# Kernel optimization log

Measured on AMD Instinct MI355X. Metric: run time of the kernel, lower is better.

The kernel has to match this reference:

```python
import jax, jax.numpy as jnp
import numpy as np
import math

D_MODEL, N_HEADS, D_HEAD = 768, 12, 64
INIT_RANGE = 0.02
ROPE_BASE = 10000.0


def _rope_cos_sin(seq_len, d_head, dtype=jnp.float32):
    # theta_j = base^(-2j/d), positions m -> angles [T, d/2]
    inv_freq = 1.0 / (ROPE_BASE ** (jnp.arange(0, d_head, 2, dtype=jnp.float32) / d_head))
    ang = jnp.arange(seq_len, dtype=jnp.float32)[:, None] * inv_freq[None, :]
    return jnp.cos(ang).astype(dtype), jnp.sin(ang).astype(dtype)


def _apply_rope(x, cos, sin):
    # x: [b, t, h, d]; rotate consecutive (even, odd) pairs as complex numbers
    xr, xi = x[..., 0::2], x[..., 1::2]
    c = cos[None, :, None, :]
    s = sin[None, :, None, :]
    out_r = xr * c - xi * s
    out_i = xr * s + xi * c
    return jnp.stack([out_r, out_i], axis=-1).reshape(x.shape)


def setup_inputs() -> dict:
    key = jax.random.key(0)
    ks = jax.random.split(key, 5)
    B, T = 2, 2048
    x = jax.random.normal(ks[0], (B, T, D_MODEL), dtype=jnp.float32)
    W_Q = INIT_RANGE * jax.random.normal(ks[1], (N_HEADS, D_MODEL, D_HEAD), dtype=jnp.float32)
    W_K = INIT_RANGE * jax.random.normal(ks[2], (N_HEADS, D_MODEL, D_HEAD), dtype=jnp.float32)
    W_V = INIT_RANGE * jax.random.normal(ks[3], (N_HEADS, D_MODEL, D_HEAD), dtype=jnp.float32)
    W_O = INIT_RANGE * jax.random.normal(ks[4], (N_HEADS, D_HEAD, D_MODEL), dtype=jnp.float32)
    b_Q = jnp.zeros((N_HEADS, D_HEAD), dtype=jnp.float32)
    b_K = jnp.zeros((N_HEADS, D_HEAD), dtype=jnp.float32)
    b_V = jnp.zeros((N_HEADS, D_HEAD), dtype=jnp.float32)
    b_O = jnp.zeros((D_MODEL,), dtype=jnp.float32)
    return {"normalized_resid_pre": x, "W_Q": W_Q, "b_Q": b_Q, "W_K": W_K, "b_K": b_K,
            "W_V": W_V, "b_V": b_V, "W_O": W_O, "b_O": b_O}


def reference(normalized_resid_pre, W_Q, b_Q, W_K, b_K, W_V, b_V, W_O, b_O):
    x = normalized_resid_pre
    B, T, _ = x.shape
    cos, sin = _rope_cos_sin(T, D_HEAD, x.dtype)
    Q = jnp.einsum('btc,hcd->bthd', x, W_Q) + b_Q
    K = jnp.einsum('btc,hcd->bthd', x, W_K) + b_K
    V = jnp.einsum('btc,hcd->bthd', x, W_V) + b_V
    Q = _apply_rope(Q, cos, sin)
    K = _apply_rope(K, cos, sin)
    scores = jnp.einsum('bqhd,bkhd->bhqk', Q, K) / math.sqrt(D_HEAD)
    # Faithful to source: tril zeros upper triangle, then all exact zeros -> -inf
    tril = jnp.tril(jnp.ones((T, T), dtype=bool))
    z = jnp.where(tril[None, None], scores, 0.0)
    z = jnp.where(z == 0.0, -jnp.inf, z)
    probs = jax.nn.softmax(z, axis=-1)
    o = jnp.einsum('bhqk,bkhd->bqhd', probs, V)
    return jnp.einsum('bqhd,hdm->bqm', o, W_O) + b_O
```

## Files before the change

### kernel.cpp

```cpp
#include <hip/hip_runtime.h>

typedef unsigned short u16;
typedef unsigned int u32;
typedef short bf16x8 __attribute__((ext_vector_type(8)));
typedef float f32x4 __attribute__((ext_vector_type(4)));
typedef float f32x16 __attribute__((ext_vector_type(16)));

#define MFMA(a, b, c) __builtin_amdgcn_mfma_f32_16x16x32_bf16(a, b, c, 0, 0, 0)
#define MFMA32(a, b, c) __builtin_amdgcn_mfma_f32_32x32x16_bf16(a, b, c, 0, 0, 0)

__device__ __forceinline__ u16 f2bf(float f) {
  unsigned int u = __float_as_uint(f);
  u = (u + 0x7FFFu + ((u >> 16) & 1u)) >> 16;
  return (u16)u;
}

#define GLOAD16(gp, lp)                                                        \
  __builtin_amdgcn_global_load_lds(                                            \
      (const __attribute__((address_space(1))) void*)(gp),                     \
      (__attribute__((address_space(3))) void*)(lp), 16, 0, 0)


__global__ void rope_tables(float* __restrict__ cost, float* __restrict__ sint) {
  int idx = blockIdx.x * 256 + threadIdx.x;
  if (idx >= 2048 * 32) return;
  int t = idx >> 5, i = idx & 31;
  float invf = expf(-(float)i * 0.28782313662425572f);
  float ang = (float)t * invf;
  cost[idx] = cosf(ang);
  sint[idx] = sinf(ang);
}

__global__ void cast_x(const float* __restrict__ x, u16* __restrict__ xb, int n) {
  int i = (blockIdx.x * 256 + threadIdx.x) * 4;
  if (i >= n) return;
  float4 v = *(const float4*)(x + i);
  u16 o0 = f2bf(v.x), o1 = f2bf(v.y), o2 = f2bf(v.z), o3 = f2bf(v.w);
  ushort4 o = make_ushort4(o0, o1, o2, o3);
  *(ushort4*)(xb + i) = o;
}

__global__ void prep_wqkv(const float* __restrict__ WQ, const float* __restrict__ WK,
                          const float* __restrict__ WV, u16* __restrict__ Wt) {
  __shared__ float tile[32][33];
  const int z = blockIdx.z;
  const int qkv = z / 12, h = z - qkv * 12;
  const float* W = (qkv == 0 ? WQ : qkv == 1 ? WK : WV) + (size_t)h * 768 * 64;
  const int k0 = blockIdx.x * 32, d0 = blockIdx.y * 32;
  const int tx = threadIdx.x, ty = threadIdx.y;
#pragma unroll
  for (int it = 0; it < 4; it++)
    tile[ty + it * 8][tx] = W[(size_t)(k0 + ty + it * 8) * 64 + d0 + tx];
  __syncthreads();
  u16* out = Wt + (size_t)(qkv * 768 + h * 64 + d0) * 768 + k0;
#pragma unroll
  for (int it = 0; it < 4; it++)
    out[(size_t)(ty + it * 8) * 768 + tx] = f2bf(tile[tx][ty + it * 8]);
}

__global__ void prep_wo(const float* __restrict__ WO, u16* __restrict__ Wt) {
  __shared__ float tile[32][33];
  const int a0 = blockIdx.x * 32, m0 = blockIdx.y * 32;
  const int tx = threadIdx.x, ty = threadIdx.y;
#pragma unroll
  for (int it = 0; it < 4; it++)
    tile[ty + it * 8][tx] = WO[(size_t)(a0 + ty + it * 8) * 768 + m0 + tx];
  __syncthreads();
#pragma unroll
  for (int it = 0; it < 4; it++)
    Wt[(size_t)(m0 + ty + it * 8) * 768 + a0 + tx] = f2bf(tile[tx][ty + it * 8]);
}

template <int MODE>
__global__ __launch_bounds__(256) void gemm_bt(
    const u16* __restrict__ A, const u16* __restrict__ Bt, int K, int LDA, int LDB,
    const float* __restrict__ bQ, const float* __restrict__ bK, const float* __restrict__ bV,
    const float* __restrict__ cost, const float* __restrict__ sint,
    u16* __restrict__ Qb, u16* __restrict__ Kb, u16* __restrict__ Vt,
    const float* __restrict__ bO, float* __restrict__ Out) {
  __shared__ u16 As[3][128 * 32];
  __shared__ u16 Bs[3][128 * 32];
  const int tid = threadIdx.x;
  const int w = tid >> 6, l = tid & 63;
  const int lr = l >> 4, lc = l & 15;
  const int wr = w >> 1, wc = w & 1;

  const int id = blockIdx.x + (int)gridDim.x * blockIdx.y;
  const int xcd = id & 7, idx = id >> 3;
  const int m0 = (xcd * 4 + (idx & 3)) * 128;
  const int n0 = (idx >> 2) * 128;

  f32x4 acc[4][4];
#pragma unroll
  for (int mi = 0; mi < 4; mi++)
#pragma unroll
    for (int ni = 0; ni < 4; ni++) acc[mi][ni] = (f32x4){0.f, 0.f, 0.f, 0.f};

  const int srow = w * 16 + (l >> 2);
  const int sg = (l & 3) ^ ((l >> 3) & 3);
  const u16* ga = A + (size_t)(m0 + srow) * LDA + sg * 8;
  const u16* gb = Bt + (size_t)(n0 + srow) * LDB + sg * 8;

#define GSTAGE(t, bi)                                                   \
  {                                                                     \
    const int kk = (t) * 32;                                            \
    GLOAD16(ga + kk, &As[bi][w * 512]);                                 \
    GLOAD16(ga + kk + (size_t)64 * LDA, &As[bi][2048 + w * 512]);       \
    GLOAD16(gb + kk, &Bs[bi][w * 512]);                                 \
    GLOAD16(gb + kk + (size_t)64 * LDB, &Bs[bi][2048 + w * 512]);       \
  }

  const int n = K >> 5;
  GSTAGE(0, 0);
  if (n > 1) GSTAGE(1, 1);

  for (int kt = 0; kt < n; kt++) {
    if (kt + 1 < n) asm volatile("s_waitcnt vmcnt(4)" ::: "memory");
    else            asm volatile("s_waitcnt vmcnt(0)" ::: "memory");
    __builtin_amdgcn_s_barrier();
    __builtin_amdgcn_sched_barrier(0);
    if (kt + 2 < n) GSTAGE(kt + 2, (kt + 2) % 3);

    const char* as = (const char*)As[kt % 3];
    const char* bs = (const char*)Bs[kt % 3];
    bf16x8 af[4], bfr[4];
#pragma unroll
    for (int mi = 0; mi < 4; mi++) {
      const int row = wr * 64 + mi * 16 + lc;
      af[mi] = *(const bf16x8*)(as + row * 64 + ((lr ^ ((row >> 1) & 3)) << 4));
    }
#pragma unroll
    for (int ni = 0; ni < 4; ni++) {
      const int row = wc * 64 + ni * 16 + lc;
      bfr[ni] = *(const bf16x8*)(bs + row * 64 + ((lr ^ ((row >> 1) & 3)) << 4));
    }
    __builtin_amdgcn_s_setprio(1);
#pragma unroll
    for (int mi = 0; mi < 4; mi++)
#pragma unroll
      for (int ni = 0; ni < 4; ni++)
        acc[mi][ni] = MFMA(af[mi], bfr[ni], acc[mi][ni]);
    __builtin_amdgcn_s_setprio(0);
  }
#undef GSTAGE

#pragma unroll
  for (int mi = 0; mi < 4; mi++) {
#pragma unroll
    for (int ni = 0; ni < 4; ni++) {
      const int col = n0 + wc * 64 + ni * 16 + lc;
      const int rowb = m0 + wr * 64 + mi * 16 + lr * 4;
      if (MODE == 0) {
        const int qkv = col / 768;
        const int rem = col - qkv * 768;
        const int h = rem >> 6, d = rem & 63, fi = d >> 1;
        const float bb = (qkv == 0 ? bQ : qkv == 1 ? bK : bV)[rem];
#pragma unroll
        for (int r = 0; r < 4; r++) {
          const int grow = rowb + r;
          const int t = grow & 2047;
          float v = acc[mi][ni][r] + bb;
          float pv = __shfl_xor(v, 1);
          if (qkv < 2) {
            const float c = cost[t * 32 + fi], s = sint[t * 32 + fi];
            float o = (d & 1) ? (pv * s + v * c) : (v * c - pv * s);
            if (qkv == 0) o *= 0.125f;
            (qkv == 0 ? Qb : Kb)[(size_t)grow * 768 + rem] = f2bf(o);
          } else {
            const int bidx = grow >> 11;
            Vt[((size_t)(bidx * 12 + h) * 64 + d) * 2048 + t] = f2bf(v);
          }
        }
      } else {
        const float bb = bO[col];
#pragma unroll
        for (int r = 0; r < 4; r++) {
          const int grow = rowb + r;
          Out[(size_t)grow * 768 + col] = acc[mi][ni][r] + bb;
        }
      }
    }
  }
}

__global__ __launch_bounds__(256, 2) void attn_kernel(
    const u16* __restrict__ Qb, const u16* __restrict__ Kb,
    const u16* __restrict__ Vt, u16* __restrict__ Ob) {
  __shared__ char Kls[4][8192];
  __shared__ char Vls[4][8192];
  char* scratch = (char*)Kls;

  const int id = blockIdx.x + 16 * blockIdx.y;
  const int s_ = id >> 3;
  const int bh = (id & 7) + 8 * (s_ % 3);
  const int xq = s_ / 3;
  const int b = bh / 12, h = bh - b * 12;
  const int tid = threadIdx.x, w = tid >> 6, l = tid & 63;
  const int lq = l & 31, hi = l >> 5;
  const int qhalf = w & 1, grp = w >> 1;

  const u16* kbase = Kb + (size_t)(b * 2048) * 768 + h * 64;
  const u16* vbase = Vt + (size_t)(bh * 64) * 2048;

  const int r8 = l >> 3;
  const int scol8 = (l & 7) ^ r8;
  const u16* ksrc = kbase + (size_t)(w * 16 + r8) * 768 + scol8 * 8;
  const u16* vsrc = vbase + (size_t)(w * 16 + r8) * 2048 + scol8 * 8;

#define STAGE(t, bi)                                                        \
  {                                                                         \
    const size_t ko = (size_t)(t) * 64 * 768;                               \
    const int vo = (t) * 64;                                                \
    GLOAD16(ksrc + ko,            &Kls[bi][w * 2048]);                      \
    GLOAD16(ksrc + ko + 8 * 768,  &Kls[bi][w * 2048 + 1024]);               \
    GLOAD16(vsrc + vo,            &Vls[bi][w * 2048]);                      \
    GLOAD16(vsrc + vo + 8 * 2048, &Vls[bi][w * 2048 + 1024]);               \
  }

  const int fswz = (lq & 7) << 4;

#pragma unroll 1
  for (int half = 0; half < 2; half++) {
    const int qblk = half == 0 ? 31 - xq : xq;
    const int n = qblk + 1;
    const int nsup = (n + 1) >> 1;

    bf16x8 qf[4];
    {
      const u16* qp = Qb + ((size_t)(b * 2048 + qblk * 64 + qhalf * 32 + lq)) * 768 +
                      h * 64 + hi * 8;
#pragma unroll
      for (int c = 0; c < 4; c++) qf[c] = *(const bf16x8*)(qp + c * 16);
    }

    float m_run = -INFINITY, l_run = 0.f;
    f32x16 acc2[2];
    acc2[0] = (f32x16)0.0f;
    acc2[1] = (f32x16)0.0f;

    STAGE(0, 0);
    if (n > 1) STAGE(1, 1);

    for (int p = 0; p < nsup; p++) {
      const int t0 = 2 * p;
      asm volatile("s_waitcnt vmcnt(0)" ::: "memory");
      __builtin_amdgcn_s_barrier();
      __builtin_amdgcn_sched_barrier(0);
      if (t0 + 2 < n) STAGE(t0 + 2, (t0 + 2) & 3);
      if (t0 + 3 < n) STAGE(t0 + 3, (t0 + 3) & 3);

      const int tile = t0 + grp;
      if (tile < n) {
        const int cur = tile & 3;

        f32x16 s2[2];
        s2[0] = (f32x16)0.0f;
        s2[1] = (f32x16)0.0f;
        __builtin_amdgcn_s_setprio(1);
#pragma unroll
        for (int c = 0; c < 4; c++) {
          const int cb = (c * 32 + hi * 16) ^ fswz;
          bf16x8 kf0 = *(const bf16x8*)(&Kls[cur][lq * 128] + cb);
          bf16x8 kf1 = *(const bf16x8*)(&Kls[cur][(32 + lq) * 128] + cb);
          s2[0] = MFMA32(kf0, qf[c], s2[0]);
          s2[1] = MFMA32(kf1, qf[c], s2[1]);
        }
        __builtin_amdgcn_s_setprio(0);

        if (tile == qblk) {
          const int qrel = qhalf * 32 + lq;
#pragma unroll
          for (int kt2 = 0; kt2 < 2; kt2++)
#pragma unroll
            for (int r = 0; r < 16; r++) {
              const int ko = kt2 * 32 + (r & 3) + 8 * (r >> 2) + 4 * hi;
              if (ko > qrel) s2[kt2][r] = -INFINITY;
            }
        }

        float pm = s2[0][0];
#pragma unroll
        for (int r = 1; r < 16; r++) pm = fmaxf(pm, s2[0][r]);
#pragma unroll
        for (int r = 0; r < 16; r++) pm = fmaxf(pm, s2[1][r]);
        pm = fmaxf(pm, __shfl_xor(pm, 32));

        const float mn = fmaxf(m_run, pm);
        const float alpha = __expf(m_run - mn);
        m_run = mn;

        float rs = 0.f;
        u32 pk[2][8];
#pragma unroll
        for (int kt2 = 0; kt2 < 2; kt2++)
#pragma unroll
          for (int j = 0; j < 8; j++) {
            float p0 = __expf(s2[kt2][2 * j] - mn);
            float p1 = __expf(s2[kt2][2 * j + 1] - mn);
            rs += p0 + p1;
            asm("v_cvt_pk_bf16_f32 %0, %1, %2" : "=v"(pk[kt2][j]) : "v"(p0), "v"(p1));
          }
        l_run = l_run * alpha + rs;

        union { u32 u[4]; bf16x8 v; } pf[4];
#pragma unroll
        for (int kq = 0; kq < 4; kq++) {
          const int kt2 = kq >> 1, i0 = 4 * (kq & 1);
          u32 a0 = pk[kt2][i0], b0 = pk[kt2][i0 + 2];
          u32 a1 = pk[kt2][i0 + 1], b1 = pk[kt2][i0 + 3];
          asm("v_permlane32_swap_b32 %0, %1" : "+v"(a0), "+v"(b0));
          asm("v_permlane32_swap_b32 %0, %1" : "+v"(a1), "+v"(b1));
          pf[kq].u[0] = a0; pf[kq].u[1] = a1; pf[kq].u[2] = b0; pf[kq].u[3] = b1;
        }

#pragma unroll
        for (int dh = 0; dh < 2; dh++)
#pragma unroll
          for (int r = 0; r < 16; r++) acc2[dh][r] *= alpha;

        __builtin_amdgcn_s_setprio(1);
#pragma unroll
        for (int dh = 0; dh < 2; dh++) {
          const char* vr = &Vls[cur][(dh * 32 + lq) * 128];
#pragma unroll
          for (int kq = 0; kq < 4; kq++) {
            bf16x8 vf = *(const bf16x8*)(vr + ((kq * 32 + hi * 16) ^ fswz));
            acc2[dh] = MFMA32(vf, pf[kq].v, acc2[dh]);
          }
        }
        __builtin_amdgcn_s_setprio(0);
      }
    }

    asm volatile("s_waitcnt lgkmcnt(0)" ::: "memory");
    __builtin_amdgcn_s_barrier();
    if (grp == 1) {
      float* sc = (float*)scratch + ((size_t)(w - 2) * 64 + l) * 34;
#pragma unroll
      for (int dh = 0; dh < 2; dh++)
#pragma unroll
        for (int r = 0; r < 16; r++) sc[dh * 16 + r] = acc2[dh][r];
      sc[32] = m_run;
      sc[33] = l_run;
    }
    asm volatile("s_waitcnt lgkmcnt(0)" ::: "memory");
    __builtin_amdgcn_s_barrier();
    if (grp == 0) {
      const float* sc = (const float*)scratch + ((size_t)w * 64 + l) * 34;
      const float m1 = sc[32], l1 = sc[33];
      const float M = fmaxf(m_run, m1);
      const float a0 = __expf(m_run - M);
      const float a1 = __expf(m1 - M);
      const float lm = l_run * a0 + l1 * a1;
      const float lt = lm + __shfl_xor(lm, 32);
      const float inv = 1.0f / lt;
      u16* ob = Ob + ((size_t)(b * 2048 + qblk * 64 + qhalf * 32 + lq)) * 768 + h * 64;
#pragma unroll
      for (int dh = 0; dh < 2; dh++)
#pragma unroll
        for (int g = 0; g < 4; g++) {
          ushort4 o4;
          o4.x = f2bf((acc2[dh][4 * g + 0] * a0 + sc[dh * 16 + 4 * g + 0] * a1) * inv);
          o4.y = f2bf((acc2[dh][4 * g + 1] * a0 + sc[dh * 16 + 4 * g + 1] * a1) * inv);
          o4.z = f2bf((acc2[dh][4 * g + 2] * a0 + sc[dh * 16 + 4 * g + 2] * a1) * inv);
          o4.w = f2bf((acc2[dh][4 * g + 3] * a0 + sc[dh * 16 + 4 * g + 3] * a1) * inv);
          *(ushort4*)(ob + dh * 32 + 8 * g + 4 * hi) = o4;
        }
    }
    asm volatile("s_waitcnt lgkmcnt(0)" ::: "memory");
    __builtin_amdgcn_s_barrier();
  }
#undef STAGE
}


extern "C" void kernel_launch(void* const* d_in, const int* in_sizes, int n_in,
                              void* d_out, int out_size, void* d_ws, size_t ws_size,
                              hipStream_t stream) {
  const float* x  = (const float*)d_in[0];
  const float* WQ = (const float*)d_in[1];
  const float* bQ = (const float*)d_in[2];
  const float* WK = (const float*)d_in[3];
  const float* bK = (const float*)d_in[4];
  const float* WV = (const float*)d_in[5];
  const float* bV = (const float*)d_in[6];
  const float* WO = (const float*)d_in[7];
  const float* bO = (const float*)d_in[8];

  char* ws = (char*)d_ws;
  u16* Xb    = (u16*)(ws + 0);
  u16* Wqkv  = (u16*)(ws + 6291456);
  u16* WoT   = (u16*)(ws + 9830400);
  u16* Qb    = (u16*)(ws + 11010048);
  u16* Kb    = (u16*)(ws + 17301504);
  u16* Vt    = (u16*)(ws + 23592960);
  u16* Ob    = (u16*)(ws + 29884416);
  float* cost = (float*)(ws + 36175872);
  float* sint = (float*)(ws + 36438016);

  rope_tables<<<256, 256, 0, stream>>>(cost, sint);
  cast_x<<<3072, 256, 0, stream>>>(x, Xb, 4096 * 768);
  prep_wqkv<<<dim3(24, 2, 36), dim3(32, 8), 0, stream>>>(WQ, WK, WV, Wqkv);
  prep_wo<<<dim3(24, 24), dim3(32, 8), 0, stream>>>(WO, WoT);

  gemm_bt<0><<<dim3(32, 18), 256, 0, stream>>>(Xb, Wqkv, 768, 768, 768,
                                               bQ, bK, bV, cost, sint,
                                               Qb, Kb, Vt, nullptr, nullptr);
  attn_kernel<<<dim3(16, 24), 256, 0, stream>>>(Qb, Kb, Vt, Ob);
  gemm_bt<1><<<dim3(32, 6), 256, 0, stream>>>(Ob, WoT, 768, 768, 768,
                                              nullptr, nullptr, nullptr, nullptr, nullptr,
                                              nullptr, nullptr, nullptr, bO, (float*)d_out);
}
```

Measured before the change: 115.8 us.

## Merge prep kernels into one launch and shrink GEMM M-tile to 64 rows

Folds the four preprocessing kernels (RoPE tables, x cast, W_QKV and W_O transposes) into a single block-indexed kernel to cut launch overhead. Also halves the GEMM tile height from 128 to 64 rows, doubling block counts (1152 and 384) so more CUs are busy on the 256-CU part, at the cost of less B-tile reuse per block. The wait count drops to match the three loads issued per stage.

New measurement: 107.3 us. 7.3% less time.

```diff
diff --git a/kernel.cpp b/kernel.cpp
--- a/kernel.cpp
+++ b/kernel.cpp
@@ -20,55 +20,54 @@
       (const __attribute__((address_space(1))) void*)(gp),                     \
       (__attribute__((address_space(3))) void*)(lp), 16, 0, 0)
 
-
-__global__ void rope_tables(float* __restrict__ cost, float* __restrict__ sint) {
-  int idx = blockIdx.x * 256 + threadIdx.x;
-  if (idx >= 2048 * 32) return;
-  int t = idx >> 5, i = idx & 31;
-  float invf = expf(-(float)i * 0.28782313662425572f);
-  float ang = (float)t * invf;
-  cost[idx] = cosf(ang);
-  sint[idx] = sinf(ang);
-}
-
-__global__ void cast_x(const float* __restrict__ x, u16* __restrict__ xb, int n) {
-  int i = (blockIdx.x * 256 + threadIdx.x) * 4;
-  if (i >= n) return;
-  float4 v = *(const float4*)(x + i);
-  u16 o0 = f2bf(v.x), o1 = f2bf(v.y), o2 = f2bf(v.z), o3 = f2bf(v.w);
-  ushort4 o = make_ushort4(o0, o1, o2, o3);
-  *(ushort4*)(xb + i) = o;
-}
-
-__global__ void prep_wqkv(const float* __restrict__ WQ, const float* __restrict__ WK,
-                          const float* __restrict__ WV, u16* __restrict__ Wt) {
+__global__ __launch_bounds__(256) void prep_all(
+    const float* __restrict__ x, const float* __restrict__ WQ,
+    const float* __restrict__ WK, const float* __restrict__ WV,
+    const float* __restrict__ WO, float* __restrict__ cost, float* __restrict__ sint,
+    u16* __restrict__ xb, u16* __restrict__ Wt, u16* __restrict__ WoT) {
   __shared__ float tile[32][33];
-  const int z = blockIdx.z;
-  const int qkv = z / 12, h = z - qkv * 12;
-  const float* W = (qkv == 0 ? WQ : qkv == 1 ? WK : WV) + (size_t)h * 768 * 64;
-  const int k0 = blockIdx.x * 32, d0 = blockIdx.y * 32;
-  const int tx = threadIdx.x, ty = threadIdx.y;
-#pragma unroll
-  for (int it = 0; it < 4; it++)
-    tile[ty + it * 8][tx] = W[(size_t)(k0 + ty + it * 8) * 64 + d0 + tx];
-  __syncthreads();
-  u16* out = Wt + (size_t)(qkv * 768 + h * 64 + d0) * 768 + k0;
-#pragma unroll
-  for (int it = 0; it < 4; it++)
-    out[(size_t)(ty + it * 8) * 768 + tx] = f2bf(tile[tx][ty + it * 8]);
-}
-
-__global__ void prep_wo(const float* __restrict__ WO, u16* __restrict__ Wt) {
-  __shared__ float tile[32][33];
-  const int a0 = blockIdx.x * 32, m0 = blockIdx.y * 32;
-  const int tx = threadIdx.x, ty = threadIdx.y;
-#pragma unroll
-  for (int it = 0; it < 4; it++)
-    tile[ty + it * 8][tx] = WO[(size_t)(a0 + ty + it * 8) * 768 + m0 + tx];
-  __syncthreads();
-#pragma unroll
-  for (int it = 0; it < 4; it++)
-    Wt[(size_t)(m0 + ty + it * 8) * 768 + a0 + tx] = f2bf(tile[tx][ty + it * 8]);
+  const int bid = blockIdx.x, tid = threadIdx.x;
+
+  if (bid < 256) {
+    int idx = bid * 256 + tid;
+    int t = idx >> 5, i = idx & 31;
+    float invf = expf(-(float)i * 0.28782313662425572f);
+    float ang = (float)t * invf;
+    cost[idx] = cosf(ang);
+    sint[idx] = sinf(ang);
+  } else if (bid < 3328) {
+    int i = ((bid - 256) * 256 + tid) * 4;
+    float4 v = *(const float4*)(x + i);
+    ushort4 o = make_ushort4(f2bf(v.x), f2bf(v.y), f2bf(v.z), f2bf(v.w));
+    *(ushort4*)(xb + i) = o;
+  } else if (bid < 5056) {
+    const int pbid = bid - 3328;
+    const int z = pbid / 48, rem = pbid - z * 48;
+    const int y = rem / 24, xk = rem - y * 24;
+    const int qkv = z / 12, h = z - qkv * 12;
+    const float* W = (qkv == 0 ? WQ : qkv == 1 ? WK : WV) + (size_t)h * 768 * 64;
+    const int k0 = xk * 32, d0 = y * 32;
+    const int tx = tid & 31, ty = tid >> 5;
+#pragma unroll
+    for (int it = 0; it < 4; it++)
+      tile[ty + it * 8][tx] = W[(size_t)(k0 + ty + it * 8) * 64 + d0 + tx];
+    __syncthreads();
+    u16* out = Wt + (size_t)(qkv * 768 + h * 64 + d0) * 768 + k0;
+#pragma unroll
+    for (int it = 0; it < 4; it++)
+      out[(size_t)(ty + it * 8) * 768 + tx] = f2bf(tile[tx][ty + it * 8]);
+  } else {
+    const int wbid = bid - 5056;
+    const int a0 = (wbid % 24) * 32, m0 = (wbid / 24) * 32;
+    const int tx = tid & 31, ty = tid >> 5;
+#pragma unroll
+    for (int it = 0; it < 4; it++)
+      tile[ty + it * 8][tx] = WO[(size_t)(a0 + ty + it * 8) * 768 + m0 + tx];
+    __syncthreads();
+#pragma unroll
+    for (int it = 0; it < 4; it++)
+      WoT[(size_t)(m0 + ty + it * 8) * 768 + a0 + tx] = f2bf(tile[tx][ty + it * 8]);
+  }
 }
 
 template <int MODE>
@@ -78,21 +77,21 @@
     const float* __restrict__ cost, const float* __restrict__ sint,
     u16* __restrict__ Qb, u16* __restrict__ Kb, u16* __restrict__ Vt,
     const float* __restrict__ bO, float* __restrict__ Out) {
-  __shared__ u16 As[3][128 * 32];
+  __shared__ u16 As[3][64 * 32];
   __shared__ u16 Bs[3][128 * 32];
   const int tid = threadIdx.x;
   const int w = tid >> 6, l = tid & 63;
   const int lr = l >> 4, lc = l & 15;
   const int wr = w >> 1, wc = w & 1;
 
-  const int id = blockIdx.x + (int)gridDim.x * blockIdx.y;
+  const int id = blockIdx.x;
   const int xcd = id & 7, idx = id >> 3;
-  const int m0 = (xcd * 4 + (idx & 3)) * 128;
-  const int n0 = (idx >> 2) * 128;
-
-  f32x4 acc[4][4];
-#pragma unroll
-  for (int mi = 0; mi < 4; mi++)
+  const int m0 = (xcd * 8 + (idx & 7)) * 64;
+  const int n0 = (idx >> 3) * 128;
+
+  f32x4 acc[2][4];
+#pragma unroll
+  for (int mi = 0; mi < 2; mi++)
 #pragma unroll
     for (int ni = 0; ni < 4; ni++) acc[mi][ni] = (f32x4){0.f, 0.f, 0.f, 0.f};
 
@@ -105,7 +104,6 @@
   {                                                                     \
     const int kk = (t) * 32;                                            \
     GLOAD16(ga + kk, &As[bi][w * 512]);                                 \
-    GLOAD16(ga + kk + (size_t)64 * LDA, &As[bi][2048 + w * 512]);       \
     GLOAD16(gb + kk, &Bs[bi][w * 512]);                                 \
     GLOAD16(gb + kk + (size_t)64 * LDB, &Bs[bi][2048 + w * 512]);       \
   }
@@ -115,7 +113,7 @@
   if (n > 1) GSTAGE(1, 1);
 
   for (int kt = 0; kt < n; kt++) {
-    if (kt + 1 < n) asm volatile("s_waitcnt vmcnt(4)" ::: "memory");
+    if (kt + 1 < n) asm volatile("s_waitcnt vmcnt(3)" ::: "memory");
     else            asm volatile("s_waitcnt vmcnt(0)" ::: "memory");
     __builtin_amdgcn_s_barrier();
     __builtin_amdgcn_sched_barrier(0);
@@ -123,10 +121,10 @@
 
     const char* as = (const char*)As[kt % 3];
     const char* bs = (const char*)Bs[kt % 3];
-    bf16x8 af[4], bfr[4];
-#pragma unroll
-    for (int mi = 0; mi < 4; mi++) {
-      const int row = wr * 64 + mi * 16 + lc;
+    bf16x8 af[2], bfr[4];
+#pragma unroll
+    for (int mi = 0; mi < 2; mi++) {
+      const int row = wr * 32 + mi * 16 + lc;
       af[mi] = *(const bf16x8*)(as + row * 64 + ((lr ^ ((row >> 1) & 3)) << 4));
     }
 #pragma unroll
@@ -136,7 +134,7 @@
     }
     __builtin_amdgcn_s_setprio(1);
 #pragma unroll
-    for (int mi = 0; mi < 4; mi++)
+    for (int mi = 0; mi < 2; mi++)
 #pragma unroll
       for (int ni = 0; ni < 4; ni++)
         acc[mi][ni] = MFMA(af[mi], bfr[ni], acc[mi][ni]);
@@ -145,11 +143,11 @@
 #undef GSTAGE
 
 #pragma unroll
-  for (int mi = 0; mi < 4; mi++) {
+  for (int mi = 0; mi < 2; mi++) {
 #pragma unroll
     for (int ni = 0; ni < 4; ni++) {
       const int col = n0 + wc * 64 + ni * 16 + lc;
-      const int rowb = m0 + wr * 64 + mi * 16 + lr * 4;
+      const int rowb = m0 + wr * 32 + mi * 16 + lr * 4;
       if (MODE == 0) {
         const int qkv = col / 768;
         const int rem = col - qkv * 768;
@@ -398,16 +396,13 @@
   float* cost = (float*)(ws + 36175872);
   float* sint = (float*)(ws + 36438016);
 
-  rope_tables<<<256, 256, 0, stream>>>(cost, sint);
-  cast_x<<<3072, 256, 0, stream>>>(x, Xb, 4096 * 768);
-  prep_wqkv<<<dim3(24, 2, 36), dim3(32, 8), 0, stream>>>(WQ, WK, WV, Wqkv);
-  prep_wo<<<dim3(24, 24), dim3(32, 8), 0, stream>>>(WO, WoT);
-
-  gemm_bt<0><<<dim3(32, 18), 256, 0, stream>>>(Xb, Wqkv, 768, 768, 768,
-                                               bQ, bK, bV, cost, sint,
-                                               Qb, Kb, Vt, nullptr, nullptr);
+  prep_all<<<5632, 256, 0, stream>>>(x, WQ, WK, WV, WO, cost, sint, Xb, Wqkv, WoT);
+
+  gemm_bt<0><<<1152, 256, 0, stream>>>(Xb, Wqkv, 768, 768, 768,
+                                       bQ, bK, bV, cost, sint,
+                                       Qb, Kb, Vt, nullptr, nullptr);
   attn_kernel<<<dim3(16, 24), 256, 0, stream>>>(Qb, Kb, Vt, Ob);
-  gemm_bt<1><<<dim3(32, 6), 256, 0, stream>>>(Ob, WoT, 768, 768, 768,
-                                              nullptr, nullptr, nullptr, nullptr, nullptr,
-                                              nullptr, nullptr, nullptr, bO, (float*)d_out);
+  gemm_bt<1><<<384, 256, 0, stream>>>(Ob, WoT, 768, 768, 768,
+                                      nullptr, nullptr, nullptr, nullptr, nullptr,
+                                      nullptr, nullptr, nullptr, bO, (float*)d_out);
 }
```
